# Kernel optimization log

Measured on AMD Instinct MI355X. Metric: run time of the kernel, lower is better.

Reference implementation:

```python
import jax, jax.numpy as jnp
import numpy as np

# ---- static config (from module __init__ defaults) ----
INPUT_DIM = 3
NUM_LEVELS = 16
LEVEL_DIM = 2
SCALE = 2.0
BASE_RES = 16
LOG2_T = 19
MAX_T = 2 ** LOG2_T
NUM_FREQS = 6
N_POINTS = 2_000_000
PRIMES = np.array([1, 2654435761, 805459861], dtype=np.uint32)  # Instant-NGP spatial hash primes
CORNERS = np.array([[i, j, k] for i in (0, 1) for j in (0, 1) for k in (0, 1)], dtype=np.int32)  # [8,3]

RES = [int(np.floor(BASE_RES * SCALE ** l)) for l in range(NUM_LEVELS)]
SIZES = [min(MAX_T, (r + 1) ** 3) for r in RES]  # dense if the full grid fits in the hashmap
OFFSETS = np.concatenate([[0], np.cumsum(SIZES)]).astype(np.int64)
TOTAL = int(OFFSETS[-1])  # 7,131,219 rows


def setup_inputs() -> dict:
    key = jax.random.key(0)
    k1, k2 = jax.random.split(key)
    x = jax.random.uniform(k1, (N_POINTS, INPUT_DIM), dtype=jnp.float32)  # points in [0,1]^3
    # hash-grid features init U(-1e-4, 1e-4) as in Instant-NGP
    table = (jax.random.uniform(k2, (TOTAL, LEVEL_DIM), dtype=jnp.float32) * 2.0 - 1.0) * 1e-4
    return {"x": x, "table": table}


def _level_interp(x, table_l, res, size):
    """Trilinear hash-grid interpolation at one level. x:[N,3] in [0,1]."""
    pos = x * jnp.float32(res)            # [N,3]
    p0f = jnp.floor(pos)
    frac = pos - p0f                      # [N,3]
    p0 = p0f.astype(jnp.int32)
    corners = jnp.clip(p0[:, None, :] + CORNERS[None], 0, res)  # [N,8,3], grid has res+1 verts
    if (res + 1) ** 3 <= MAX_T:
        # dense stride indexing
        r1 = res + 1
        idx = corners[..., 0] + corners[..., 1] * r1 + corners[..., 2] * (r1 * r1)
    else:
        c = corners.astype(jnp.uint32)
        h = (c[..., 0] * jnp.uint32(int(PRIMES[0]))
             ^ c[..., 1] * jnp.uint32(int(PRIMES[1]))
             ^ c[..., 2] * jnp.uint32(int(PRIMES[2])))
        idx = (h % jnp.uint32(size)).astype(jnp.int32)
    vals = table_l[idx]                   # [N,8,level_dim] gather
    # trilinear weights: prod over dims of (frac if corner==1 else 1-frac)
    w = jnp.where(CORNERS[None] == 1, frac[:, None, :], 1.0 - frac[:, None, :]).prod(-1)  # [N,8]
    return jnp.einsum('nc,ncd->nd', w, vals)  # [N,level_dim]


def _hash_encode(x, table):
    feats = [
        _level_interp(x, table[int(OFFSETS[l]):int(OFFSETS[l + 1])], RES[l], SIZES[l])
        for l in range(NUM_LEVELS)
    ]
    return jnp.concatenate(feats, axis=-1)  # [N, num_levels*level_dim]


def _pos_encode(x):
    coeffs = jnp.float32(2.0) ** jnp.arange(NUM_FREQS, dtype=jnp.float32)  # log_sampling
    xc = x[:, None, :] * coeffs[None, :, None]           # [N,F,3]
    sc = jnp.stack([jnp.sin(xc), jnp.cos(xc)], axis=2)   # [N,F,2,3] -> order: per-freq sin(3) then cos(3)
    return jnp.concatenate([x, sc.reshape(x.shape[0], 2 * NUM_FREQS * INPUT_DIM)], axis=-1)


def reference(x, table):
    hash_feat = _hash_encode(x, table)   # [N,32]
    freq_feat = _pos_encode(x)           # [N,39]
    return jnp.concatenate([hash_feat, freq_feat], axis=-1)  # [N,71]
```

## Files before the change

kernel.cpp:

```cpp
#include <hip/hip_runtime.h>

typedef float f4 __attribute__((ext_vector_type(4)));

#define BLK 128
#define NLEV 16
#define NHASH 13
#define HSIZE 524288
#define HMASK 524287u
#define KOFF3 315475
#define SROW 36
#define CONV_BLOCKS ((NHASH * HSIZE) / 256)

__constant__ int kOff[NLEV] = {0, 4913, 40850, 315475, 839763, 1364051, 1888339,
                               2412627, 2936915, 3461203, 3985491, 4509779,
                               5034067, 5558355, 6082643, 6606931};

__global__ __launch_bounds__(256)
void prep_kernel(const float* __restrict__ xs, const float2* __restrict__ tab,
                 unsigned* __restrict__ tbf, f4* __restrict__ xs4, int n)
{
    const int b = blockIdx.x;
    if (b < CONV_BLOCKS) {
        const int i = b * 256 + threadIdx.x;
        float2 v = tab[KOFF3 + i];
        tbf[i] = (__float_as_uint(v.x) >> 16) | (__float_as_uint(v.y) & 0xFFFF0000u);
    } else {
        const int i = (b - CONV_BLOCKS) * 256 + threadIdx.x;
        if (i < n) {
            f4 p;
            p.x = xs[3 * i + 0];
            p.y = xs[3 * i + 1];
            p.z = xs[3 * i + 2];
            p.w = 0.f;
            p = p;
            xs4[i] = p;
        }
    }
}

__global__ __launch_bounds__(256)
void levels_kernel(const f4* __restrict__ xs4, const unsigned* __restrict__ tbf,
                   unsigned* __restrict__ scratch, int n)
{
    const int lev = blockIdx.y;
    const int i0  = blockIdx.x * 512 + threadIdx.x;
    const int res = 16 << (3 + lev);
    const float fres = (float)res;
    const unsigned* __restrict__ tl = tbf + (size_t)lev * HSIZE;

    unsigned hx[2], hc[2][4];
    float rx[2], ry[2], rz[2];
    bool valid[2];

    #pragma unroll
    for (int p = 0; p < 2; ++p) {
        const int i = i0 + p * 256;
        valid[p] = (i < n);
        f4 pt = {0.f, 0.f, 0.f, 0.f};
        if (valid[p]) pt = xs4[i];
        float posx = pt.x * fres, posy = pt.y * fres, posz = pt.z * fres;
        float fxf = floorf(posx), fyf = floorf(posy), fzf = floorf(posz);
        rx[p] = posx - fxf; ry[p] = posy - fyf; rz[p] = posz - fzf;
        unsigned x  = (unsigned)(int)fxf;
        unsigned y0 = (unsigned)(int)fyf * 2654435761u, y1 = y0 + 2654435761u;
        unsigned z0 = (unsigned)(int)fzf * 805459861u,  z1 = z0 + 805459861u;
        hx[p] = x;
        hc[p][0] = y0 ^ z0; hc[p][1] = y0 ^ z1; hc[p][2] = y1 ^ z0; hc[p][3] = y1 ^ z1;
    }

    unsigned va[2][4], vb[2][4];
    #pragma unroll
    for (int p = 0; p < 2; ++p) {
        #pragma unroll
        for (int c = 0; c < 4; ++c) {
            unsigned ia = (hx[p] ^ hc[p][c]) & HMASK;
            uint2 q = *(const uint2*)(tl + (ia & ~1u));
            va[p][c] = (ia & 1u) ? q.y : q.x;
            vb[p][c] = (ia & 1u) ? q.x : q.y;
        }
    }
    #pragma unroll
    for (int p = 0; p < 2; ++p) {
        if (hx[p] & 1u) {
            unsigned x1 = hx[p] + 1u;
            #pragma unroll
            for (int c = 0; c < 4; ++c)
                vb[p][c] = tl[(x1 ^ hc[p][c]) & HMASK];
        }
    }

    #pragma unroll
    for (int p = 0; p < 2; ++p) {
        if (!valid[p]) continue;
        float wx1 = rx[p], wx0 = 1.f - wx1;
        float wy1 = ry[p], wy0 = 1.f - wy1;
        float wz1 = rz[p], wz0 = 1.f - wz1;
        float wc[4] = {wy0 * wz0, wy0 * wz1, wy1 * wz0, wy1 * wz1};
        float f0 = 0.f, f1 = 0.f;
        #pragma unroll
        for (int c = 0; c < 4; ++c) {
            float a0 = __uint_as_float(va[p][c] << 16);
            float a1 = __uint_as_float(va[p][c] & 0xFFFF0000u);
            float b0 = __uint_as_float(vb[p][c] << 16);
            float b1 = __uint_as_float(vb[p][c] & 0xFFFF0000u);
            f0 += wc[c] * (wx0 * a0 + wx1 * b0);
            f1 += wc[c] * (wx0 * a1 + wx1 * b1);
        }
        unsigned packed = (__float_as_uint(f0) >> 16) | (__float_as_uint(f1) & 0xFFFF0000u);
        scratch[(size_t)lev * n + (i0 + p * 256)] = packed;
    }
}

__global__ __launch_bounds__(256)
void levels_f32_kernel(const float* __restrict__ xs, const float2* __restrict__ tab,
                       unsigned* __restrict__ scratch, int n)
{
    const int lev = blockIdx.y;
    const int i   = blockIdx.x * 256 + threadIdx.x;
    if (i >= n) return;
    const int res = 16 << (3 + lev);
    const float2* __restrict__ tl = tab + kOff[3 + lev];

    const float px = xs[3 * i + 0];
    const float py = xs[3 * i + 1];
    const float pz = xs[3 * i + 2];

    const float fres = (float)res;
    float posx = px * fres, posy = py * fres, posz = pz * fres;
    float fxf = floorf(posx), fyf = floorf(posy), fzf = floorf(posz);
    float rx = posx - fxf, ry = posy - fyf, rz = posz - fzf;

    unsigned hx  = (unsigned)(int)fxf;
    unsigned hy0 = (unsigned)(int)fyf * 2654435761u, hy1 = hy0 + 2654435761u;
    unsigned hz0 = (unsigned)(int)fzf * 805459861u,  hz1 = hz0 + 805459861u;
    unsigned h00 = hy0 ^ hz0, h01 = hy0 ^ hz1, h10 = hy1 ^ hz0, h11 = hy1 ^ hz1;

    unsigned hx1 = hx + 1u;
    float2 v000 = tl[(hx ^ h00) & HMASK], v100 = tl[(hx1 ^ h00) & HMASK];
    float2 v001 = tl[(hx ^ h01) & HMASK], v101 = tl[(hx1 ^ h01) & HMASK];
    float2 v010 = tl[(hx ^ h10) & HMASK], v110 = tl[(hx1 ^ h10) & HMASK];
    float2 v011 = tl[(hx ^ h11) & HMASK], v111 = tl[(hx1 ^ h11) & HMASK];

    float wx1 = rx, wx0 = 1.f - rx;
    float wy1 = ry, wy0 = 1.f - ry;
    float wz1 = rz, wz0 = 1.f - rz;

    float f0, f1, w;
    w = wx0 * wy0 * wz0; f0  = w * v000.x; f1  = w * v000.y;
    w = wx0 * wy0 * wz1; f0 += w * v001.x; f1 += w * v001.y;
    w = wx0 * wy1 * wz0; f0 += w * v010.x; f1 += w * v010.y;
    w = wx0 * wy1 * wz1; f0 += w * v011.x; f1 += w * v011.y;
    w = wx1 * wy0 * wz0; f0 += w * v100.x; f1 += w * v100.y;
    w = wx1 * wy0 * wz1; f0 += w * v101.x; f1 += w * v101.y;
    w = wx1 * wy1 * wz0; f0 += w * v110.x; f1 += w * v110.y;
    w = wx1 * wy1 * wz1; f0 += w * v111.x; f1 += w * v111.y;

    unsigned packed = (__float_as_uint(f0) >> 16) | (__float_as_uint(f1) & 0xFFFF0000u);
    scratch[(size_t)lev * n + i] = packed;
}

__global__ __launch_bounds__(BLK)
void final_kernel(const f4* __restrict__ xs4, const float* __restrict__ table,
                  const unsigned* __restrict__ scratch, float* __restrict__ out, int n)
{
    __shared__ float sbuf[BLK * SROW];
    const int tid  = threadIdx.x;
    const int base = blockIdx.x * BLK;
    const int pi   = base + tid;
    const bool val = (pi < n);

    unsigned sc[NHASH];
    if (val) {
        #pragma unroll
        for (int h = 0; h < NHASH; ++h)
            sc[h] = scratch[(size_t)h * n + pi];
    }

    f4 pt = {0.f, 0.f, 0.f, 0.f};
    if (val) pt = xs4[pi];
    const float px = pt.x, py = pt.y, pz = pt.z;

    float* srow = sbuf + tid * SROW;
    const float2* __restrict__ tab = (const float2*)table;

    #pragma unroll
    for (int l = 0; l < 3; ++l) {
        const int res = 16 << l;
        const float2* __restrict__ tl = tab + kOff[l];
        const float fres = (float)res;

        float posx = px * fres, posy = py * fres, posz = pz * fres;
        float fxf = floorf(posx), fyf = floorf(posy), fzf = floorf(posz);
        float rx = posx - fxf, ry = posy - fyf, rz = posz - fzf;

        const unsigned r1 = (unsigned)(res + 1);
        const unsigned r2 = r1 * r1;
        unsigned x0 = (unsigned)(int)fxf;
        unsigned by0 = (unsigned)(int)fyf * r1; unsigned by1 = by0 + r1;
        unsigned cz0 = (unsigned)(int)fzf * r2; unsigned cz1 = cz0 + r2;

        float2 v000, v001, v010, v011, v100, v101, v110, v111;
        #define PAIRD(B, VA, VB) { \
            unsigned i0 = x0 + (B); \
            if ((i0 & 1u) == 0u) { f4 q = *(const f4*)(tl + i0); \
                VA.x = q.x; VA.y = q.y; VB.x = q.z; VB.y = q.w; } \
            else { VA = tl[i0]; VB = tl[i0 + 1u]; } }
        PAIRD(by0 + cz0, v000, v100)
        PAIRD(by0 + cz1, v001, v101)
        PAIRD(by1 + cz0, v010, v110)
        PAIRD(by1 + cz1, v011, v111)
        #undef PAIRD

        float wx1 = rx, wx0 = 1.f - rx;
        float wy1 = ry, wy0 = 1.f - ry;
        float wz1 = rz, wz0 = 1.f - rz;

        float f0, f1, w;
        w = wx0 * wy0 * wz0; f0  = w * v000.x; f1  = w * v000.y;
        w = wx0 * wy0 * wz1; f0 += w * v001.x; f1 += w * v001.y;
        w = wx0 * wy1 * wz0; f0 += w * v010.x; f1 += w * v010.y;
        w = wx0 * wy1 * wz1; f0 += w * v011.x; f1 += w * v011.y;
        w = wx1 * wy0 * wz0; f0 += w * v100.x; f1 += w * v100.y;
        w = wx1 * wy0 * wz1; f0 += w * v101.x; f1 += w * v101.y;
        w = wx1 * wy1 * wz0; f0 += w * v110.x; f1 += w * v110.y;
        w = wx1 * wy1 * wz1; f0 += w * v111.x; f1 += w * v111.y;

        srow[2 * l]     = f0;
        srow[2 * l + 1] = f1;
    }

    #pragma unroll
    for (int h = 0; h < NHASH; ++h) {
        srow[6 + 2 * h] = __uint_as_float(sc[h] << 16);
        srow[7 + 2 * h] = __uint_as_float(sc[h] & 0xFFFF0000u);
    }
    srow[32] = px; srow[33] = py; srow[34] = pz;

    __syncthreads();

    const int nvalid = min(BLK, n - base);
    float* obase = out + (size_t)base * 71;
    if (nvalid == BLK) {
        f4* o4 = (f4*)obase;
        #pragma unroll 1
        for (int i = tid; i < (BLK * 71) / 4; i += BLK) {
            const int e = 4 * i;
            f4 v;
            #pragma unroll
            for (int j = 0; j < 4; ++j) {
                const int ee = e + j;
                const int p = ee / 71;
                const int f = ee - p * 71;
                float valf;
                if (f < 35) {
                    valf = sbuf[p * SROW + f];
                } else {
                    const int g = f - 35;
                    const int freq = g / 6;
                    const int r = g - 6 * freq;
                    const int dim = (r < 3) ? r : r - 3;
                    const float a = sbuf[p * SROW + 32 + dim] * (float)(1 << freq);
                    float s, c;
                    __sincosf(a, &s, &c);
                    valf = (r < 3) ? s : c;
                }
                v[j] = valf;
            }
            __builtin_nontemporal_store(v, &o4[i]);
        }
    } else {
        #pragma unroll 1
        for (int i = tid; i < nvalid * 71; i += BLK) {
            const int p = i / 71;
            const int f = i - p * 71;
            float valf;
            if (f < 35) {
                valf = sbuf[p * SROW + f];
            } else {
                const int g = f - 35;
                const int freq = g / 6;
                const int r = g - 6 * freq;
                const int dim = (r < 3) ? r : r - 3;
                const float a = sbuf[p * SROW + 32 + dim] * (float)(1 << freq);
                float s, c;
                __sincosf(a, &s, &c);
                valf = (r < 3) ? s : c;
            }
            __builtin_nontemporal_store(valf, &obase[i]);
        }
    }
}

__global__ __launch_bounds__(BLK)
void final_f32_kernel(const float* __restrict__ xs, const float* __restrict__ table,
                      const unsigned* __restrict__ scratch, float* __restrict__ out, int n)
{
    __shared__ float sbuf[BLK * SROW];
    const int tid  = threadIdx.x;
    const int base = blockIdx.x * BLK;
    const int pi   = base + tid;

    float px = 0.f, py = 0.f, pz = 0.f;
    if (pi < n) { px = xs[3*pi]; py = xs[3*pi+1]; pz = xs[3*pi+2]; }

    float* srow = sbuf + tid * SROW;
    const float2* __restrict__ tab = (const float2*)table;

    #pragma unroll
    for (int l = 0; l < 3; ++l) {
        const int res = 16 << l;
        const float2* __restrict__ tl = tab + kOff[l];
        const float fres = (float)res;
        float posx = px * fres, posy = py * fres, posz = pz * fres;
        float fxf = floorf(posx), fyf = floorf(posy), fzf = floorf(posz);
        float rx = posx - fxf, ry = posy - fyf, rz = posz - fzf;
        const unsigned r1 = (unsigned)(res + 1), r2 = r1 * r1;
        unsigned x0 = (unsigned)(int)fxf;
        unsigned by0 = (unsigned)(int)fyf * r1, by1 = by0 + r1;
        unsigned cz0 = (unsigned)(int)fzf * r2, cz1 = cz0 + r2;
        float2 v000 = tl[x0+by0+cz0], v100 = tl[x0+by0+cz0+1];
        float2 v001 = tl[x0+by0+cz1], v101 = tl[x0+by0+cz1+1];
        float2 v010 = tl[x0+by1+cz0], v110 = tl[x0+by1+cz0+1];
        float2 v011 = tl[x0+by1+cz1], v111 = tl[x0+by1+cz1+1];
        float wx1 = rx, wx0 = 1.f - rx, wy1 = ry, wy0 = 1.f - ry, wz1 = rz, wz0 = 1.f - rz;
        float f0, f1, w;
        w = wx0*wy0*wz0; f0  = w*v000.x; f1  = w*v000.y;
        w = wx0*wy0*wz1; f0 += w*v001.x; f1 += w*v001.y;
        w = wx0*wy1*wz0; f0 += w*v010.x; f1 += w*v010.y;
        w = wx0*wy1*wz1; f0 += w*v011.x; f1 += w*v011.y;
        w = wx1*wy0*wz0; f0 += w*v100.x; f1 += w*v100.y;
        w = wx1*wy0*wz1; f0 += w*v101.x; f1 += w*v101.y;
        w = wx1*wy1*wz0; f0 += w*v110.x; f1 += w*v110.y;
        w = wx1*wy1*wz1; f0 += w*v111.x; f1 += w*v111.y;
        srow[2*l] = f0; srow[2*l+1] = f1;
    }
    if (pi < n) {
        #pragma unroll
        for (int h = 0; h < NHASH; ++h) {
            unsigned u = scratch[(size_t)h * n + pi];
            srow[6+2*h] = __uint_as_float(u << 16);
            srow[7+2*h] = __uint_as_float(u & 0xFFFF0000u);
        }
    }
    srow[32] = px; srow[33] = py; srow[34] = pz;
    __syncthreads();
    const int nvalid = min(BLK, n - base);
    float* obase = out + (size_t)base * 71;
    #pragma unroll 1
    for (int i = tid; i < nvalid * 71; i += BLK) {
        const int p = i / 71;
        const int f = i - p * 71;
        float valf;
        if (f < 35) {
            valf = sbuf[p * SROW + f];
        } else {
            const int g = f - 35;
            const int freq = g / 6;
            const int r = g - 6 * freq;
            const int dim = (r < 3) ? r : r - 3;
            const float a = sbuf[p * SROW + 32 + dim] * (float)(1 << freq);
            float s, c;
            __sincosf(a, &s, &c);
            valf = (r < 3) ? s : c;
        }
        __builtin_nontemporal_store(valf, &obase[i]);
    }
}

extern "C" void kernel_launch(void* const* d_in, const int* in_sizes, int n_in,
                              void* d_out, int out_size, void* d_ws, size_t ws_size,
                              hipStream_t stream) {
    const float* xs    = (const float*)d_in[0];
    const float* table = (const float*)d_in[1];
    float* out = (float*)d_out;
    const int n = in_sizes[0] / 3;

    unsigned* scratch = (unsigned*)d_ws;
    const size_t featBytes = (size_t)NHASH * (size_t)n * 4u;
    const size_t tblBytes  = (size_t)NHASH * HSIZE * 4u;
    const size_t xs4Bytes  = (size_t)n * 16u;
    const float2* tab = (const float2*)table;
    const int gf = (n + BLK - 1) / BLK;

    if (ws_size >= featBytes + tblBytes + xs4Bytes) {
        unsigned* tbf = (unsigned*)((char*)d_ws + featBytes);
        f4* xs4 = (f4*)((char*)d_ws + featBytes + tblBytes);

        const int packBlocks = (n + 255) / 256;
        hipLaunchKernelGGL(prep_kernel, dim3(CONV_BLOCKS + packBlocks), dim3(256),
                           0, stream, xs, tab, tbf, xs4, n);

        const int bpl = (n + 511) / 512;
        hipLaunchKernelGGL(levels_kernel, dim3(bpl, NHASH), dim3(256), 0, stream,
                           xs4, tbf, scratch, n);
        hipLaunchKernelGGL(final_kernel, dim3(gf), dim3(BLK), 0, stream,
                           xs4, table, scratch, out, n);
    } else {
        const int bpl = (n + 255) / 256;
        hipLaunchKernelGGL(levels_f32_kernel, dim3(bpl, NHASH), dim3(256), 0, stream,
                           xs, tab, scratch, n);
        hipLaunchKernelGGL(final_f32_kernel, dim3(gf), dim3(BLK), 0, stream,
                           xs, table, scratch, out, n);
    }
}
```

Baseline: 777.6 us.

## Move positional encoding into levels kernel and split output writes

After: 888.7 us. 14.3% more time.

```diff
diff --git a/kernel.cpp b/kernel.cpp
--- a/kernel.cpp
+++ b/kernel.cpp
@@ -32,7 +32,6 @@
             p.y = xs[3 * i + 1];
             p.z = xs[3 * i + 2];
             p.w = 0.f;
-            p = p;
             xs4[i] = p;
         }
     }
@@ -40,13 +39,19 @@
 
 __global__ __launch_bounds__(256)
 void levels_kernel(const f4* __restrict__ xs4, const unsigned* __restrict__ tbf,
-                   unsigned* __restrict__ scratch, int n)
-{
-    const int lev = blockIdx.y;
-    const int i0  = blockIdx.x * 512 + threadIdx.x;
+                   unsigned* __restrict__ scratch, float* __restrict__ out,
+                   int n, int bpl, int ppb)
+{
+    const int tid = threadIdx.x;
+    const int bid = blockIdx.x;
+    const int lev = bid / bpl;
+    const int xq  = bid - lev * bpl;
+    const int i0  = xq * 512 + tid;
     const int res = 16 << (3 + lev);
     const float fres = (float)res;
     const unsigned* __restrict__ tl = tbf + (size_t)lev * HSIZE;
+
+    __shared__ float pl[40][40];
 
     unsigned hx[2], hc[2][4];
     float rx[2], ry[2], rz[2];
@@ -109,63 +114,46 @@
         unsigned packed = (__float_as_uint(f0) >> 16) | (__float_as_uint(f1) & 0xFFFF0000u);
         scratch[(size_t)lev * n + (i0 + p * 256)] = packed;
     }
+
+    const int pp0 = bid * ppb;
+    if (tid < 120) {
+        const int p = tid / 3, d = tid - 3 * p;
+        const int pt = pp0 + p;
+        if (p < ppb && pt < n) {
+            f4 q = xs4[pt];
+            float coord = (d == 0) ? q.x : (d == 1) ? q.y : q.z;
+            pl[p][d] = coord;
+            float s, c;
+            __sincosf(coord, &s, &c);
+            #pragma unroll
+            for (int fr = 0; fr < 6; ++fr) {
+                pl[p][3 + 6 * fr + d]     = s;
+                pl[p][3 + 6 * fr + 3 + d] = c;
+                if (fr < 5) {
+                    float ns = 2.f * s * c, nc = 1.f - 2.f * s * s;
+                    s = ns; c = nc;
+                }
+            }
+        }
+    }
+    __syncthreads();
+    const int tot = ppb * 39;
+    #pragma unroll 1
+    for (int i = tid; i < tot; i += 256) {
+        const int p = i / 39, j = i - 39 * p;
+        const int pt = pp0 + p;
+        if (pt < n)
+            __builtin_nontemporal_store(pl[p][j], &out[(size_t)pt * 71 + 32 + j]);
+    }
 }
 
 __global__ __launch_bounds__(256)
-void levels_f32_kernel(const float* __restrict__ xs, const float2* __restrict__ tab,
-                       unsigned* __restrict__ scratch, int n)
-{
-    const int lev = blockIdx.y;
-    const int i   = blockIdx.x * 256 + threadIdx.x;
-    if (i >= n) return;
-    const int res = 16 << (3 + lev);
-    const float2* __restrict__ tl = tab + kOff[3 + lev];
-
-    const float px = xs[3 * i + 0];
-    const float py = xs[3 * i + 1];
-    const float pz = xs[3 * i + 2];
-
-    const float fres = (float)res;
-    float posx = px * fres, posy = py * fres, posz = pz * fres;
-    float fxf = floorf(posx), fyf = floorf(posy), fzf = floorf(posz);
-    float rx = posx - fxf, ry = posy - fyf, rz = posz - fzf;
-
-    unsigned hx  = (unsigned)(int)fxf;
-    unsigned hy0 = (unsigned)(int)fyf * 2654435761u, hy1 = hy0 + 2654435761u;
-    unsigned hz0 = (unsigned)(int)fzf * 805459861u,  hz1 = hz0 + 805459861u;
-    unsigned h00 = hy0 ^ hz0, h01 = hy0 ^ hz1, h10 = hy1 ^ hz0, h11 = hy1 ^ hz1;
-
-    unsigned hx1 = hx + 1u;
-    float2 v000 = tl[(hx ^ h00) & HMASK], v100 = tl[(hx1 ^ h00) & HMASK];
-    float2 v001 = tl[(hx ^ h01) & HMASK], v101 = tl[(hx1 ^ h01) & HMASK];
-    float2 v010 = tl[(hx ^ h10) & HMASK], v110 = tl[(hx1 ^ h10) & HMASK];
-    float2 v011 = tl[(hx ^ h11) & HMASK], v111 = tl[(hx1 ^ h11) & HMASK];
-
-    float wx1 = rx, wx0 = 1.f - rx;
-    float wy1 = ry, wy0 = 1.f - ry;
-    float wz1 = rz, wz0 = 1.f - rz;
-
-    float f0, f1, w;
-    w = wx0 * wy0 * wz0; f0  = w * v000.x; f1  = w * v000.y;
-    w = wx0 * wy0 * wz1; f0 += w * v001.x; f1 += w * v001.y;
-    w = wx0 * wy1 * wz0; f0 += w * v010.x; f1 += w * v010.y;
-    w = wx0 * wy1 * wz1; f0 += w * v011.x; f1 += w * v011.y;
-    w = wx1 * wy0 * wz0; f0 += w * v100.x; f1 += w * v100.y;
-    w = wx1 * wy0 * wz1; f0 += w * v101.x; f1 += w * v101.y;
-    w = wx1 * wy1 * wz0; f0 += w * v110.x; f1 += w * v110.y;
-    w = wx1 * wy1 * wz1; f0 += w * v111.x; f1 += w * v111.y;
-
-    unsigned packed = (__float_as_uint(f0) >> 16) | (__float_as_uint(f1) & 0xFFFF0000u);
-    scratch[(size_t)lev * n + i] = packed;
-}
-
-__global__ __launch_bounds__(BLK)
-void final_kernel(const f4* __restrict__ xs4, const float* __restrict__ table,
+void merge_kernel(const f4* __restrict__ xs4, const float* __restrict__ table,
                   const unsigned* __restrict__ scratch, float* __restrict__ out, int n)
 {
-    __shared__ float sbuf[BLK * SROW];
+    __shared__ float mb[256][32];
     const int tid  = threadIdx.x;
-    const int base = blockIdx.x * BLK;
+    const int base = blockIdx.x * 256;
     const int pi   = base + tid;
     const bool val = (pi < n);
 
@@ -179,8 +167,6 @@
     f4 pt = {0.f, 0.f, 0.f, 0.f};
     if (val) pt = xs4[pi];
     const float px = pt.x, py = pt.y, pz = pt.z;
-
-    float* srow = sbuf + tid * SROW;
     const float2* __restrict__ tab = (const float2*)table;
 
     #pragma unroll
@@ -225,70 +211,72 @@
         w = wx1 * wy1 * wz0; f0 += w * v110.x; f1 += w * v110.y;
         w = wx1 * wy1 * wz1; f0 += w * v111.x; f1 += w * v111.y;
 
-        srow[2 * l]     = f0;
-        srow[2 * l + 1] = f1;
+        mb[tid][2 * l]     = f0;
+        mb[tid][2 * l + 1] = f1;
     }
 
     #pragma unroll
     for (int h = 0; h < NHASH; ++h) {
-        srow[6 + 2 * h] = __uint_as_float(sc[h] << 16);
-        srow[7 + 2 * h] = __uint_as_float(sc[h] & 0xFFFF0000u);
-    }
-    srow[32] = px; srow[33] = py; srow[34] = pz;
+        mb[tid][6 + 2 * h] = __uint_as_float(sc[h] << 16);
+        mb[tid][7 + 2 * h] = __uint_as_float(sc[h] & 0xFFFF0000u);
+    }
 
     __syncthreads();
 
-    const int nvalid = min(BLK, n - base);
-    float* obase = out + (size_t)base * 71;
-    if (nvalid == BLK) {
-        f4* o4 = (f4*)obase;
-        #pragma unroll 1
-        for (int i = tid; i < (BLK * 71) / 4; i += BLK) {
-            const int e = 4 * i;
-            f4 v;
-            #pragma unroll
-            for (int j = 0; j < 4; ++j) {
-                const int ee = e + j;
-                const int p = ee / 71;
-                const int f = ee - p * 71;
-                float valf;
-                if (f < 35) {
-                    valf = sbuf[p * SROW + f];
-                } else {
-                    const int g = f - 35;
-                    const int freq = g / 6;
-                    const int r = g - 6 * freq;
-                    const int dim = (r < 3) ? r : r - 3;
-                    const float a = sbuf[p * SROW + 32 + dim] * (float)(1 << freq);
-                    float s, c;
-                    __sincosf(a, &s, &c);
-                    valf = (r < 3) ? s : c;
-                }
-                v[j] = valf;
-            }
-            __builtin_nontemporal_store(v, &o4[i]);
-        }
-    } else {
-        #pragma unroll 1
-        for (int i = tid; i < nvalid * 71; i += BLK) {
-            const int p = i / 71;
-            const int f = i - p * 71;
-            float valf;
-            if (f < 35) {
-                valf = sbuf[p * SROW + f];
-            } else {
-                const int g = f - 35;
-                const int freq = g / 6;
-                const int r = g - 6 * freq;
-                const int dim = (r < 3) ? r : r - 3;
-                const float a = sbuf[p * SROW + 32 + dim] * (float)(1 << freq);
-                float s, c;
-                __sincosf(a, &s, &c);
-                valf = (r < 3) ? s : c;
-            }
-            __builtin_nontemporal_store(valf, &obase[i]);
-        }
-    }
+    #pragma unroll 1
+    for (int i = tid; i < 256 * 32; i += 256) {
+        const int p = i >> 5, c = i & 31;
+        if (base + p < n)
+            __builtin_nontemporal_store(mb[p][c], &out[(size_t)(base + p) * 71 + c]);
+    }
+}
+
+__global__ __launch_bounds__(256)
+void levels_f32_kernel(const float* __restrict__ xs, const float2* __restrict__ tab,
+                       unsigned* __restrict__ scratch, int n)
+{
+    const int lev = blockIdx.y;
+    const int i   = blockIdx.x * 256 + threadIdx.x;
+    if (i >= n) return;
+    const int res = 16 << (3 + lev);
+    const float2* __restrict__ tl = tab + kOff[3 + lev];
+
+    const float px = xs[3 * i + 0];
+    const float py = xs[3 * i + 1];
+    const float pz = xs[3 * i + 2];
+
+    const float fres = (float)res;
+    float posx = px * fres, posy = py * fres, posz = pz * fres;
+    float fxf = floorf(posx), fyf = floorf(posy), fzf = floorf(posz);
+    float rx = posx - fxf, ry = posy - fyf, rz = posz - fzf;
+
+    unsigned hx  = (unsigned)(int)fxf;
+    unsigned hy0 = (unsigned)(int)fyf * 2654435761u, hy1 = hy0 + 2654435761u;
+    unsigned hz0 = (unsigned)(int)fzf * 805459861u,  hz1 = hz0 + 805459861u;
+    unsigned h00 = hy0 ^ hz0, h01 = hy0 ^ hz1, h10 = hy1 ^ hz0, h11 = hy1 ^ hz1;
+
+    unsigned hx1 = hx + 1u;
+    float2 v000 = tl[(hx ^ h00) & HMASK], v100 = tl[(hx1 ^ h00) & HMASK];
+    float2 v001 = tl[(hx ^ h01) & HMASK], v101 = tl[(hx1 ^ h01) & HMASK];
+    float2 v010 = tl[(hx ^ h10) & HMASK], v110 = tl[(hx1 ^ h10) & HMASK];
+    float2 v011 = tl[(hx ^ h11) & HMASK], v111 = tl[(hx1 ^ h11) & HMASK];
+
+    float wx1 = rx, wx0 = 1.f - rx;
+    float wy1 = ry, wy0 = 1.f - ry;
+    float wz1 = rz, wz0 = 1.f - rz;
+
+    float f0, f1, w;
+    w = wx0 * wy0 * wz0; f0  = w * v000.x; f1  = w * v000.y;
+    w = wx0 * wy0 * wz1; f0 += w * v001.x; f1 += w * v001.y;
+    w = wx0 * wy1 * wz0; f0 += w * v010.x; f1 += w * v010.y;
+    w = wx0 * wy1 * wz1; f0 += w * v011.x; f1 += w * v011.y;
+    w = wx1 * wy0 * wz0; f0 += w * v100.x; f1 += w * v100.y;
+    w = wx1 * wy0 * wz1; f0 += w * v101.x; f1 += w * v101.y;
+    w = wx1 * wy1 * wz0; f0 += w * v110.x; f1 += w * v110.y;
+    w = wx1 * wy1 * wz1; f0 += w * v111.x; f1 += w * v111.y;
+
+    unsigned packed = (__float_as_uint(f0) >> 16) | (__float_as_uint(f1) & 0xFFFF0000u);
+    scratch[(size_t)lev * n + i] = packed;
 }
 
 __global__ __launch_bounds__(BLK)
@@ -380,7 +368,6 @@
     const size_t tblBytes  = (size_t)NHASH * HSIZE * 4u;
     const size_t xs4Bytes  = (size_t)n * 16u;
     const float2* tab = (const float2*)table;
-    const int gf = (n + BLK - 1) / BLK;
 
     if (ws_size >= featBytes + tblBytes + xs4Bytes) {
         unsigned* tbf = (unsigned*)((char*)d_ws + featBytes);
@@ -391,14 +378,19 @@
                            0, stream, xs, tab, tbf, xs4, n);
 
         const int bpl = (n + 511) / 512;
-        hipLaunchKernelGGL(levels_kernel, dim3(bpl, NHASH), dim3(256), 0, stream,
-                           xs4, tbf, scratch, n);
-        hipLaunchKernelGGL(final_kernel, dim3(gf), dim3(BLK), 0, stream,
+        const int nb  = NHASH * bpl;
+        const int ppb = (n + nb - 1) / nb;
+        hipLaunchKernelGGL(levels_kernel, dim3(nb), dim3(256), 0, stream,
+                           xs4, tbf, scratch, out, n, bpl, ppb);
+
+        const int gm = (n + 255) / 256;
+        hipLaunchKernelGGL(merge_kernel, dim3(gm), dim3(256), 0, stream,
                            xs4, table, scratch, out, n);
     } else {
         const int bpl = (n + 255) / 256;
         hipLaunchKernelGGL(levels_f32_kernel, dim3(bpl, NHASH), dim3(256), 0, stream,
                            xs, tab, scratch, n);
+        const int gf = (n + BLK - 1) / BLK;
         hipLaunchKernelGGL(final_f32_kernel, dim3(gf), dim3(BLK), 0, stream,
                            xs, table, scratch, out, n);
     }
```
